# Kernel optimization log

Measured on AMD Instinct MI355X. Metric: run time of the kernel, lower is better.

The kernel has to match this reference:

```python
import jax, jax.numpy as jnp
from jax import lax
import numpy as np

NEG_SLOPE = 0.01  # torch leaky_relu default
KSIZE = 5

def lrelu(x):
    return jax.nn.leaky_relu(x, NEG_SLOPE)

def conv(x, w, b):
    # x: [N,C,H,W], w: [O,I,kh,kw], valid padding (pad=False in ConvChain)
    y = lax.conv_general_dilated(x, w, (1, 1), 'VALID',
                                 dimension_numbers=('NCHW', 'OIHW', 'NCHW'))
    return y + b[None, :, None, None]

def _forward(features, radiance, global_features,
             emb_w0, emb_b0, emb_w, emb_b,
             pf_w0, pf_b0, pf_w1, pf_b1, pf_w2, pf_b2,
             sf_w, sf_b,
             kp_w0, kp_b0, kp_w1, kp_b1, kp_w2, kp_b2):
    bs, spp, nf, h, w = features.shape
    ngf = global_features.shape[1]
    K = KSIZE

    # --- sample_embedding over all samples at once (replaces per-sp loop) ---
    g = jnp.broadcast_to(global_features, (bs, ngf, h, w))
    x = jnp.concatenate(
        [jnp.broadcast_to(g[:, None], (bs, spp, ngf, h, w)), features], axis=2)
    x = x.reshape(bs * spp, ngf + nf, h, w)
    x = lrelu(conv(x, emb_w0, emb_b0))
    for i in range(5):  # hidden conv layers 1..5
        x = lrelu(conv(x, emb_w[i], emb_b[i]))
    x = conv(x, emb_w[5], emb_b[5])  # linear output layer
    pixel_embed = x.reshape(bs, spp, x.shape[1], x.shape[2], x.shape[3]).max(axis=1)

    # --- pixel_features chain (3 layers, last linear) ---
    p = lrelu(conv(pixel_embed, pf_w0, pf_b0))
    p = lrelu(conv(p, pf_w1, pf_b1))
    pfeat = conv(p, pf_w2, pf_b2)  # [bs, pair_width, ph, pw]
    ph, pw = pfeat.shape[2], pfeat.shape[3]

    # --- crop features/radiance so needed = ph + K - 1 ---
    needed = ph + K - 1
    crop = (h - needed) // 2
    feat_c = features[..., crop:crop + needed, crop:crop + needed]
    rad_c = radiance[..., crop:crop + needed, crop:crop + needed]

    # --- gather K*K taps per pixel (unfold) ---
    taps = jnp.stack([feat_c[..., dy:dy + ph, dx:dx + pw]
                      for dy in range(K) for dx in range(K)], axis=0)
    # [K,K,bs,spp,nf,ph,pw] -> [bs,ph,pw,spp,ky,kx,nf]
    taps = taps.reshape(K, K, bs, spp, nf, ph, pw).transpose(2, 5, 6, 3, 0, 1, 4)
    off = jnp.arange(K, dtype=taps.dtype) - K // 2
    taps = taps.at[..., 0].add(off)            # x += kx - K//2 (kx axis)
    taps = taps.at[..., 1].add(off[:, None])   # y += ky - K//2 (ky axis)

    rt = jnp.stack([rad_c[..., dy:dy + ph, dx:dx + pw]
                    for dy in range(K) for dx in range(K)], axis=0)
    # [K,K,bs,spp,3,ph,pw] -> [bs,3,ph,pw,spp,ky,kx]
    rt = rt.reshape(K, K, bs, spp, 3, ph, pw).transpose(2, 4, 5, 6, 3, 0, 1)

    # --- sample_features: single linear layer (FullyConnected depth=1) ---
    sf = jnp.einsum('...f,of->...o', taps, sf_w) + sf_b  # [b,ph,pw,spp,ky,kx,pair]

    # --- kernel_predictor on pixel_features + sample_features ---
    pairf = pfeat.transpose(0, 2, 3, 1)[:, :, :, None, None, None, :]
    hdd = lrelu(jnp.einsum('...i,oi->...o', pairf + sf, kp_w0) + kp_b0)
    hdd = lrelu(jnp.einsum('...i,oi->...o', hdd, kp_w1) + kp_b1)
    wts = (jnp.einsum('...i,oi->...o', hdd, kp_w2) + kp_b2)[..., 0]  # [b,ph,pw,spp,ky,kx]

    # --- weighted radiance accumulate + normalize ---
    unnorm = jnp.einsum('bhwsyx,bchwsyx->bchw', wts, rt)
    sumw = wts.sum(axis=(3, 4, 5))[:, None]  # [b,1,ph,pw]
    return unnorm / (sumw + 1e-8)


def setup_inputs() -> dict:
    key = jax.random.key(0)
    ks = jax.random.split(key, 24)
    BS, SPP, NF, NGF, H, W = 1, 4, 12, 4, 116, 116
    WIDTH, PAIR = 128, 64
    s = 0.05
    inp = {}
    inp['features'] = jax.random.normal(ks[0], (BS, SPP, NF, H, W), jnp.float32)
    inp['radiance'] = jax.random.uniform(ks[1], (BS, SPP, 3, H, W), jnp.float32)
    inp['global_features'] = jax.random.normal(ks[2], (BS, NGF, 1, 1), jnp.float32)
    # sample_embedding: 7 conv layers (first 16->128, rest 128->128, last linear)
    inp['emb_w0'] = jax.random.normal(ks[3], (WIDTH, NF + NGF, 3, 3)) * s
    inp['emb_b0'] = jax.random.normal(ks[4], (WIDTH,)) * s
    inp['emb_w'] = jax.random.normal(ks[5], (6, WIDTH, WIDTH, 3, 3)) * s
    inp['emb_b'] = jax.random.normal(ks[6], (6, WIDTH)) * s
    # pixel_features: 3 conv layers 128->128->128->64 (last linear)
    inp['pf_w0'] = jax.random.normal(ks[7], (WIDTH, WIDTH, 3, 3)) * s
    inp['pf_b0'] = jax.random.normal(ks[8], (WIDTH,)) * s
    inp['pf_w1'] = jax.random.normal(ks[9], (WIDTH, WIDTH, 3, 3)) * s
    inp['pf_b1'] = jax.random.normal(ks[10], (WIDTH,)) * s
    inp['pf_w2'] = jax.random.normal(ks[11], (PAIR, WIDTH, 3, 3)) * s
    inp['pf_b2'] = jax.random.normal(ks[12], (PAIR,)) * s
    # sample_features: FullyConnected(12 -> 64, depth=1) = single linear
    inp['sf_w'] = jax.random.normal(ks[13], (PAIR, NF)) * s
    inp['sf_b'] = jax.random.normal(ks[14], (PAIR,)) * s
    # kernel_predictor: FullyConnected(64 -> 1, depth=3)
    inp['kp_w0'] = jax.random.normal(ks[15], (PAIR, PAIR)) * s
    inp['kp_b0'] = jax.random.normal(ks[16], (PAIR,)) * s
    inp['kp_w1'] = jax.random.normal(ks[17], (PAIR, PAIR)) * s
    inp['kp_b1'] = jax.random.normal(ks[18], (PAIR,)) * s
    inp['kp_w2'] = jax.random.normal(ks[19], (1, PAIR)) * s
    inp['kp_b2'] = jax.random.normal(ks[20], (1,)) * s
    return inp


def reference(features, radiance, global_features,
              emb_w0, emb_b0, emb_w, emb_b,
              pf_w0, pf_b0, pf_w1, pf_b1, pf_w2, pf_b2,
              sf_w, sf_b,
              kp_w0, kp_b0, kp_w1, kp_b1, kp_w2, kp_b2):
    return _forward(features, radiance, global_features,
                    emb_w0, emb_b0, emb_w, emb_b,
                    pf_w0, pf_b0, pf_w1, pf_b1, pf_w2, pf_b2,
                    sf_w, sf_b,
                    kp_w0, kp_b0, kp_w1, kp_b1, kp_w2, kp_b2)
```

## Files before the change

kernel.cpp:

```cpp
#include <hip/hip_runtime.h>


#define HW2 13456
#define NF  12
#define NGF 4

__device__ __forceinline__ float lrelu_f(float x) { return x > 0.f ? x : 0.01f * x; }

__global__ __launch_bounds__(256) void k_buildx0(const float* __restrict__ features,
                                                 const float* __restrict__ gf,
                                                 float* __restrict__ out) {
    int i = blockIdx.x * 256 + threadIdx.x;
    const int total = 4 * 16 * HW2;
    if (i >= total) return;
    int n  = i / (16 * HW2);
    int r  = i - n * (16 * HW2);
    int c  = r / HW2;
    int yx = r - c * HW2;
    float v = (c < NGF) ? gf[c] : features[(n * NF + (c - NGF)) * HW2 + yx];
    out[i] = v;
}

__global__ __launch_bounds__(256) void k_wt(const float* __restrict__ w,
                                            float* __restrict__ wt,
                                            int Cout, int Cin) {
    int i = blockIdx.x * 256 + threadIdx.x;
    int total = Cout * Cin * 9;
    if (i >= total) return;
    int m   = i / (Cin * 9);
    int r   = i - m * (Cin * 9);
    int cin = r / 9;
    int kyx = r - cin * 9;
    wt[(kyx * Cin + cin) * Cout + m] = w[i];
}

template <int CIN, int COUT>
__global__ __launch_bounds__(256) void k_convd(const float* __restrict__ in,
                                               const float* __restrict__ wt,
                                               const float* __restrict__ bias,
                                               float* __restrict__ out,
                                               int H, int W, int relu, int tout) {
    constexpr int MW = COUT / 4;
    const int OH = H - 2, OW = W - 2;
    const int n   = blockIdx.z;
    const int ty0 = blockIdx.y * 8, tx0 = blockIdx.x * 8;

    __shared__ float It[CIN * 100];

    const int tid = threadIdx.x;

    const float* inb = in + (size_t)n * CIN * H * W;
    for (int i = tid; i < CIN * 100; i += 256) {
        int cin = i / 100;
        int r   = i - cin * 100;
        int y   = r / 10;
        int x   = r - y * 10;
        int gy = ty0 + y; if (gy > H - 1) gy = H - 1;
        int gx = tx0 + x; if (gx > W - 1) gx = W - 1;
        It[i] = inb[((size_t)cin * H + gy) * W + gx];
    }
    __syncthreads();

    const int lane  = tid & 63;
    const int wv    = __builtin_amdgcn_readfirstlane(tid >> 6);
    const int ly    = lane >> 3, lx = lane & 7;
    const int lbase = ly * 10 + lx;

    float acc[MW];
    #pragma unroll
    for (int mi = 0; mi < MW; ++mi) acc[mi] = 0.f;

    for (int ky = 0; ky < 3; ++ky) {
        for (int kx = 0; kx < 3; ++kx) {
            const int kyx  = ky * 3 + kx;
            const int aoff = lbase + ky * 10 + kx;
            const float* wrow = wt + (size_t)kyx * CIN * COUT + wv * MW;
            #pragma unroll 8
            for (int cin = 0; cin < CIN; ++cin) {
                float v = It[cin * 100 + aoff];
                const float* wr = wrow + (size_t)cin * COUT;
                #pragma unroll
                for (int mi = 0; mi < MW; ++mi)
                    acc[mi] += wr[mi] * v;
            }
        }
    }

    int oy = ty0 + ly, ox = tx0 + lx;
    if (oy < OH && ox < OW) {
        if (tout) {
            float* ob = out + (size_t)(oy * OW + ox) * COUT;
            #pragma unroll
            for (int mi = 0; mi < MW; ++mi) {
                int m = wv * MW + mi;
                float val = acc[mi] + bias[m];
                if (relu) val = lrelu_f(val);
                ob[m] = val;
            }
        } else {
            #pragma unroll
            for (int mi = 0; mi < MW; ++mi) {
                int m = wv * MW + mi;
                float val = acc[mi] + bias[m];
                if (relu) val = lrelu_f(val);
                out[(((size_t)n * COUT + m) * OH + oy) * OW + ox] = val;
            }
        }
    }
}

__global__ __launch_bounds__(256) void k_sppmax(const float* __restrict__ in,
                                                float* __restrict__ out) {
    int i = blockIdx.x * 256 + threadIdx.x;
    const int total = 128 * 102 * 102;
    if (i >= total) return;
    float m = in[i];
    #pragma unroll
    for (int s = 1; s < 4; ++s) m = fmaxf(m, in[i + s * total]);
    out[i] = m;
}

__global__ __launch_bounds__(128) void k_mlp(const float* __restrict__ features,
                                             const float* __restrict__ pfeat_t,
                                             const float* __restrict__ sf_w,
                                             const float* __restrict__ sf_b,
                                             const float* __restrict__ w0, const float* __restrict__ b0,
                                             const float* __restrict__ w1, const float* __restrict__ b1,
                                             const float* __restrict__ w2, const float* __restrict__ b2,
                                             float* __restrict__ wts) {
    __shared__ float vx[64][128];
    const int t   = threadIdx.x;
    const int gid = blockIdx.x * 128 + t;
    int p  = gid / 100;
    int r  = gid - p * 100;
    int s  = r / 25;
    int tp = r - s * 25;
    int dy = tp / 5;
    int dx = tp - dy * 5;
    int h  = p / 96;
    int w  = p - h * 96;

    int y = 8 + h + dy, x = 8 + w + dx;
    const float* fb = features + (size_t)(s * NF) * HW2 + (size_t)y * 116 + x;
    float f[12];
    #pragma unroll
    for (int i = 0; i < 12; ++i) f[i] = fb[i * HW2];
    f[0] += (float)(dx - 2);
    f[1] += (float)(dy - 2);

    const float* pft = pfeat_t + (size_t)p * 64;
    float v[64];
    #pragma unroll
    for (int o = 0; o < 64; ++o) {
        float a = 0.f;
        #pragma unroll
        for (int i = 0; i < 12; ++i) a += sf_w[o * 12 + i] * f[i];
        a += sf_b[o];
        v[o] = pft[o] + a;
    }

    #pragma unroll 1
    for (int ob = 0; ob < 64; ob += 8) {
        float acc[8];
        #pragma unroll
        for (int j = 0; j < 8; ++j) acc[j] = 0.f;
        #pragma unroll
        for (int i = 0; i < 64; ++i) {
            float vi = v[i];
            #pragma unroll
            for (int j = 0; j < 8; ++j) acc[j] += w0[(ob + j) * 64 + i] * vi;
        }
        #pragma unroll
        for (int j = 0; j < 8; ++j) vx[ob + j][t] = lrelu_f(acc[j] + b0[ob + j]);
    }
    #pragma unroll
    for (int i = 0; i < 64; ++i) v[i] = vx[i][t];

    #pragma unroll 1
    for (int ob = 0; ob < 64; ob += 8) {
        float acc[8];
        #pragma unroll
        for (int j = 0; j < 8; ++j) acc[j] = 0.f;
        #pragma unroll
        for (int i = 0; i < 64; ++i) {
            float vi = v[i];
            #pragma unroll
            for (int j = 0; j < 8; ++j) acc[j] += w1[(ob + j) * 64 + i] * vi;
        }
        #pragma unroll
        for (int j = 0; j < 8; ++j) vx[ob + j][t] = lrelu_f(acc[j] + b1[ob + j]);
    }
    #pragma unroll
    for (int i = 0; i < 64; ++i) v[i] = vx[i][t];

    float a = 0.f;
    #pragma unroll
    for (int i = 0; i < 64; ++i) a += w2[i] * v[i];
    a += b2[0];
    wts[gid] = a;
}

__global__ __launch_bounds__(256) void k_reduce(const float* __restrict__ wts,
                                                const float* __restrict__ radiance,
                                                float* __restrict__ out) {
    int p = blockIdx.x * 256 + threadIdx.x;
    if (p >= 9216) return;
    int h = p / 96, w = p - h * 96;
    float sw = 0.f, un0 = 0.f, un1 = 0.f, un2 = 0.f;
    const float* wp = wts + (size_t)p * 100;
    for (int s = 0; s < 4; ++s) {
        #pragma unroll
        for (int dy = 0; dy < 5; ++dy) {
            #pragma unroll
            for (int dx = 0; dx < 5; ++dx) {
                float wv = wp[s * 25 + dy * 5 + dx];
                sw += wv;
                int y = 8 + h + dy, x = 8 + w + dx;
                const float* rb = radiance + (size_t)(s * 3) * HW2 + (size_t)y * 116 + x;
                un0 += wv * rb[0 * HW2];
                un1 += wv * rb[1 * HW2];
                un2 += wv * rb[2 * HW2];
            }
        }
    }
    float inv = 1.f / (sw + 1e-8f);
    out[0 * 9216 + p] = un0 * inv;
    out[1 * 9216 + p] = un1 * inv;
    out[2 * 9216 + p] = un2 * inv;
}

extern "C" void kernel_launch(void* const* d_in, const int* in_sizes, int n_in,
                              void* d_out, int out_size, void* d_ws, size_t ws_size,
                              hipStream_t stream) {
    const float* features = (const float*)d_in[0];
    const float* radiance = (const float*)d_in[1];
    const float* gf       = (const float*)d_in[2];
    const float* emb_w0   = (const float*)d_in[3];
    const float* emb_b0   = (const float*)d_in[4];
    const float* emb_w    = (const float*)d_in[5];
    const float* emb_b    = (const float*)d_in[6];
    const float* pf_w0    = (const float*)d_in[7];
    const float* pf_b0    = (const float*)d_in[8];
    const float* pf_w1    = (const float*)d_in[9];
    const float* pf_b1    = (const float*)d_in[10];
    const float* pf_w2    = (const float*)d_in[11];
    const float* pf_b2    = (const float*)d_in[12];
    const float* sf_w     = (const float*)d_in[13];
    const float* sf_b     = (const float*)d_in[14];
    const float* kp_w0    = (const float*)d_in[15];
    const float* kp_b0    = (const float*)d_in[16];
    const float* kp_w1    = (const float*)d_in[17];
    const float* kp_b1    = (const float*)d_in[18];
    const float* kp_w2    = (const float*)d_in[19];
    const float* kp_b2    = (const float*)d_in[20];
    float* out = (float*)d_out;

    float* WT = (float*)d_ws;
    float* wt0  = WT;
    float* wtE0 = WT + 18432;
    float* wtP0 = WT + 18432 + 6 * 147456;
    float* wtP1 = WT + 1050624;
    float* wtP2 = WT + 1198080;
    float* A = WT + 1271808;
    float* B = A + 6653952;

    auto wtr = [&](const float* w, float* dst, int Cout, int Cin) {
        int total = Cout * Cin * 9;
        k_wt<<<dim3((total + 255) / 256), 256, 0, stream>>>(w, dst, Cout, Cin);
    };
    wtr(emb_w0, wt0, 128, 16);
    for (int i = 0; i < 6; ++i) wtr(emb_w + i * 147456, wtE0 + i * 147456, 128, 128);
    wtr(pf_w0, wtP0, 128, 128);
    wtr(pf_w1, wtP1, 128, 128);
    wtr(pf_w2, wtP2, 64, 128);

    k_buildx0<<<dim3((4 * 16 * HW2 + 255) / 256), 256, 0, stream>>>(features, gf, A);

    auto grid8 = [](int OH, int OW, int N) {
        return dim3((OW + 7) / 8, (OH + 7) / 8, N);
    };

    k_convd<16, 128><<<grid8(114, 114, 4), 256, 0, stream>>>(A, wt0, emb_b0, B, 116, 116, 1, 0);
    k_convd<128,128><<<grid8(112, 112, 4), 256, 0, stream>>>(B, wtE0 + 0*147456, emb_b + 0*128, A, 114, 114, 1, 0);
    k_convd<128,128><<<grid8(110, 110, 4), 256, 0, stream>>>(A, wtE0 + 1*147456, emb_b + 1*128, B, 112, 112, 1, 0);
    k_convd<128,128><<<grid8(108, 108, 4), 256, 0, stream>>>(B, wtE0 + 2*147456, emb_b + 2*128, A, 110, 110, 1, 0);
    k_convd<128,128><<<grid8(106, 106, 4), 256, 0, stream>>>(A, wtE0 + 3*147456, emb_b + 3*128, B, 108, 108, 1, 0);
    k_convd<128,128><<<grid8(104, 104, 4), 256, 0, stream>>>(B, wtE0 + 4*147456, emb_b + 4*128, A, 106, 106, 1, 0);
    k_convd<128,128><<<grid8(102, 102, 4), 256, 0, stream>>>(A, wtE0 + 5*147456, emb_b + 5*128, B, 104, 104, 0, 0);

    k_sppmax<<<dim3(1331712 / 256), 256, 0, stream>>>(B, A);

    k_convd<128,128><<<grid8(100, 100, 1), 256, 0, stream>>>(A, wtP0, pf_b0, B, 102, 102, 1, 0);
    k_convd<128,128><<<grid8(98,  98,  1), 256, 0, stream>>>(B, wtP1, pf_b1, A, 100, 100, 1, 0);
    k_convd<128, 64><<<grid8(96,  96,  1), 256, 0, stream>>>(A, wtP2, pf_b2, B, 98,  98,  0, 1);

    k_mlp<<<dim3(7200), 128, 0, stream>>>(features, B, sf_w, sf_b,
                                          kp_w0, kp_b0, kp_w1, kp_b1, kp_w2, kp_b2, A);

    k_reduce<<<dim3(36), 256, 0, stream>>>(A, radiance, out);
}
```

Before: 2.905 ms.

## Retile per-tap MLP as block-cooperative register-tiled GEMM through shared memory

The kernel-predictor MLP previously had each thread run its own 64x64 matvecs, with weights read per thread. Now a 256-thread block stages 256 sample vectors in LDS, and each wavefront computes 16 output channels for 4 samples per thread. It reads float4 activations and wave-uniform weights from pre-transposed copies made by a new transpose kernel. This raises arithmetic intensity and turns weight loads into scalar/broadcast loads, at the cost of extra barriers, 64KB of LDS per block and lower occupancy.

```diff
diff --git a/kernel.cpp b/kernel.cpp
--- a/kernel.cpp
+++ b/kernel.cpp
@@ -34,6 +34,14 @@
     wt[(kyx * Cin + cin) * Cout + m] = w[i];
 }
 
+__global__ __launch_bounds__(256) void k_wt2(const float* __restrict__ w,
+                                             float* __restrict__ wt) {
+    int i = blockIdx.x * 256 + threadIdx.x;
+    if (i >= 4096) return;
+    int o = i >> 6, k = i & 63;
+    wt[k * 64 + o] = w[i];
+}
+
 template <int CIN, int COUT>
 __global__ __launch_bounds__(256) void k_convd(const float* __restrict__ in,
                                                const float* __restrict__ wt,
@@ -120,84 +128,118 @@
     out[i] = m;
 }
 
-__global__ __launch_bounds__(128) void k_mlp(const float* __restrict__ features,
+__global__ __launch_bounds__(256) void k_mlp(const float* __restrict__ features,
                                              const float* __restrict__ pfeat_t,
                                              const float* __restrict__ sf_w,
                                              const float* __restrict__ sf_b,
-                                             const float* __restrict__ w0, const float* __restrict__ b0,
-                                             const float* __restrict__ w1, const float* __restrict__ b1,
+                                             const float* __restrict__ w0t,
+                                             const float* __restrict__ b0,
+                                             const float* __restrict__ w1t,
+                                             const float* __restrict__ b1,
                                              const float* __restrict__ w2, const float* __restrict__ b2,
                                              float* __restrict__ wts) {
-    __shared__ float vx[64][128];
+    __shared__ float vx[64][256];
     const int t   = threadIdx.x;
-    const int gid = blockIdx.x * 128 + t;
-    int p  = gid / 100;
-    int r  = gid - p * 100;
-    int s  = r / 25;
-    int tp = r - s * 25;
-    int dy = tp / 5;
-    int dx = tp - dy * 5;
-    int h  = p / 96;
-    int w  = p - h * 96;
-
-    int y = 8 + h + dy, x = 8 + w + dx;
-    const float* fb = features + (size_t)(s * NF) * HW2 + (size_t)y * 116 + x;
-    float f[12];
-    #pragma unroll
-    for (int i = 0; i < 12; ++i) f[i] = fb[i * HW2];
-    f[0] += (float)(dx - 2);
-    f[1] += (float)(dy - 2);
-
-    const float* pft = pfeat_t + (size_t)p * 64;
-    float v[64];
-    #pragma unroll
-    for (int o = 0; o < 64; ++o) {
+    const int gid = blockIdx.x * 256 + t;
+    {
+        int p  = gid / 100;
+        int r  = gid - p * 100;
+        int s  = r / 25;
+        int tp = r - s * 25;
+        int dy = tp / 5;
+        int dx = tp - dy * 5;
+        int h  = p / 96;
+        int w  = p - h * 96;
+
+        int y = 8 + h + dy, x = 8 + w + dx;
+        const float* fb = features + (size_t)(s * NF) * HW2 + (size_t)y * 116 + x;
+        float f[12];
+        #pragma unroll
+        for (int i = 0; i < 12; ++i) f[i] = fb[i * HW2];
+        f[0] += (float)(dx - 2);
+        f[1] += (float)(dy - 2);
+
+        const float* pft = pfeat_t + (size_t)p * 64;
+        #pragma unroll
+        for (int o = 0; o < 64; ++o) {
+            float a = 0.f;
+            #pragma unroll
+            for (int i = 0; i < 12; ++i) a += sf_w[o * 12 + i] * f[i];
+            a += sf_b[o];
+            vx[o][t] = pft[o] + a;
+        }
+    }
+    __syncthreads();
+
+    const int lane = t & 63;
+    const int og   = 16 * __builtin_amdgcn_readfirstlane(t >> 6);
+    const int tl   = lane * 4;
+
+    {
+        float acc[16][4];
+        #pragma unroll
+        for (int j = 0; j < 16; ++j)
+            #pragma unroll
+            for (int c = 0; c < 4; ++c) acc[j][c] = 0.f;
+        #pragma unroll 4
+        for (int k = 0; k < 64; ++k) {
+            float4 xv = *(const float4*)(&vx[k][tl]);
+            const float* wr = w0t + k * 64 + og;
+            #pragma unroll
+            for (int j = 0; j < 16; ++j) {
+                float wj = wr[j];
+                acc[j][0] += wj * xv.x; acc[j][1] += wj * xv.y;
+                acc[j][2] += wj * xv.z; acc[j][3] += wj * xv.w;
+            }
+        }
+        __syncthreads();
+        #pragma unroll
+        for (int j = 0; j < 16; ++j) {
+            float bj = b0[og + j];
+            float4 ov;
+            ov.x = lrelu_f(acc[j][0] + bj); ov.y = lrelu_f(acc[j][1] + bj);
+            ov.z = lrelu_f(acc[j][2] + bj); ov.w = lrelu_f(acc[j][3] + bj);
+            *(float4*)(&vx[og + j][tl]) = ov;
+        }
+        __syncthreads();
+    }
+
+    {
+        float acc[16][4];
+        #pragma unroll
+        for (int j = 0; j < 16; ++j)
+            #pragma unroll
+            for (int c = 0; c < 4; ++c) acc[j][c] = 0.f;
+        #pragma unroll 4
+        for (int k = 0; k < 64; ++k) {
+            float4 xv = *(const float4*)(&vx[k][tl]);
+            const float* wr = w1t + k * 64 + og;
+            #pragma unroll
+            for (int j = 0; j < 16; ++j) {
+                float wj = wr[j];
+                acc[j][0] += wj * xv.x; acc[j][1] += wj * xv.y;
+                acc[j][2] += wj * xv.z; acc[j][3] += wj * xv.w;
+            }
+        }
+        __syncthreads();
+        #pragma unroll
+        for (int j = 0; j < 16; ++j) {
+            float bj = b1[og + j];
+            float4 ov;
+            ov.x = lrelu_f(acc[j][0] + bj); ov.y = lrelu_f(acc[j][1] + bj);
+            ov.z = lrelu_f(acc[j][2] + bj); ov.w = lrelu_f(acc[j][3] + bj);
+            *(float4*)(&vx[og + j][tl]) = ov;
+        }
+        __syncthreads();
+    }
+
+    {
         float a = 0.f;
         #pragma unroll
-        for (int i = 0; i < 12; ++i) a += sf_w[o * 12 + i] * f[i];
-        a += sf_b[o];
-        v[o] = pft[o] + a;
-    }
-
-    #pragma unroll 1
-    for (int ob = 0; ob < 64; ob += 8) {
-        float acc[8];
-        #pragma unroll
-        for (int j = 0; j < 8; ++j) acc[j] = 0.f;
-        #pragma unroll
-        for (int i = 0; i < 64; ++i) {
-            float vi = v[i];
-            #pragma unroll
-            for (int j = 0; j < 8; ++j) acc[j] += w0[(ob + j) * 64 + i] * vi;
-        }
-        #pragma unroll
-        for (int j = 0; j < 8; ++j) vx[ob + j][t] = lrelu_f(acc[j] + b0[ob + j]);
-    }
-    #pragma unroll
-    for (int i = 0; i < 64; ++i) v[i] = vx[i][t];
-
-    #pragma unroll 1
-    for (int ob = 0; ob < 64; ob += 8) {
-        float acc[8];
-        #pragma unroll
-        for (int j = 0; j < 8; ++j) acc[j] = 0.f;
-        #pragma unroll
-        for (int i = 0; i < 64; ++i) {
-            float vi = v[i];
-            #pragma unroll
-            for (int j = 0; j < 8; ++j) acc[j] += w1[(ob + j) * 64 + i] * vi;
-        }
-        #pragma unroll
-        for (int j = 0; j < 8; ++j) vx[ob + j][t] = lrelu_f(acc[j] + b1[ob + j]);
-    }
-    #pragma unroll
-    for (int i = 0; i < 64; ++i) v[i] = vx[i][t];
-
-    float a = 0.f;
-    #pragma unroll
-    for (int i = 0; i < 64; ++i) a += w2[i] * v[i];
-    a += b2[0];
-    wts[gid] = a;
+        for (int i = 0; i < 64; ++i) a += w2[i] * vx[i][t];
+        a += b2[0];
+        wts[gid] = a;
+    }
 }
 
 __global__ __launch_bounds__(256) void k_reduce(const float* __restrict__ wts,
@@ -261,7 +303,9 @@
     float* wtP0 = WT + 18432 + 6 * 147456;
     float* wtP1 = WT + 1050624;
     float* wtP2 = WT + 1198080;
-    float* A = WT + 1271808;
+    float* w0t  = WT + 1271808;
+    float* w1t  = WT + 1275904;
+    float* A = WT + 1280000;
     float* B = A + 6653952;
 
     auto wtr = [&](const float* w, float* dst, int Cout, int Cin) {
@@ -273,6 +317,8 @@
     wtr(pf_w0, wtP0, 128, 128);
     wtr(pf_w1, wtP1, 128, 128);
     wtr(pf_w2, wtP2, 64, 128);
+    k_wt2<<<dim3(16), 256, 0, stream>>>(kp_w0, w0t);
+    k_wt2<<<dim3(16), 256, 0, stream>>>(kp_w1, w1t);
 
     k_buildx0<<<dim3((4 * 16 * HW2 + 255) / 256), 256, 0, stream>>>(features, gf, A);
 
@@ -294,8 +340,8 @@
     k_convd<128,128><<<grid8(98,  98,  1), 256, 0, stream>>>(B, wtP1, pf_b1, A, 100, 100, 1, 0);
     k_convd<128, 64><<<grid8(96,  96,  1), 256, 0, stream>>>(A, wtP2, pf_b2, B, 98,  98,  0, 1);
 
-    k_mlp<<<dim3(7200), 128, 0, stream>>>(features, B, sf_w, sf_b,
-                                          kp_w0, kp_b0, kp_w1, kp_b1, kp_w2, kp_b2, A);
+    k_mlp<<<dim3(3600), 256, 0, stream>>>(features, B, sf_w, sf_b,
+                                          w0t, kp_b0, w1t, kp_b1, kp_w2, kp_b2, A);
 
     k_reduce<<<dim3(36), 256, 0, stream>>>(A, radiance, out);
 }
```

Result: faster. 2.643 ms (-9.0%).
